# Kernel tuning notes

Hardware: AMD Instinct MI355X
Metric: run time of the kernel (lower is better)

## Reference

```python
import jax, jax.numpy as jnp
import numpy as np


def setup_inputs() -> dict:
    key = jax.random.key(0)
    ks = jax.random.split(key, 6)
    b, l, d, n, r = 2, 2048, 512, 64, 32
    x = jax.random.normal(ks[0], (b, l, d), dtype=jnp.float32)
    # x_proj: Linear(d, r + 2n, bias=False) -> weight (r+2n, d)
    W_xproj = jax.random.normal(ks[1], (r + 2 * n, d), dtype=jnp.float32) / np.sqrt(d)
    # dt_proj: Linear(r, d, bias=True)
    W_dt = jax.random.normal(ks[2], (d, r), dtype=jnp.float32) / np.sqrt(r)
    b_dt = jax.random.normal(ks[3], (d,), dtype=jnp.float32) * 0.01
    # A_log = log(repeat(arange(1, n+1), 'n -> d n'))
    A_log = jnp.log(jnp.broadcast_to(jnp.arange(1, n + 1, dtype=jnp.float32), (d, n)))
    D = jnp.ones((d,), dtype=jnp.float32)
    return {"x": x, "W_xproj": W_xproj, "W_dt": W_dt, "b_dt": b_dt, "A_log": A_log, "D": D}


def _s6_forward(x, W_xproj, W_dt, b_dt, A_log, D):
    d, n = A_log.shape
    r = W_dt.shape[1]
    A = -jnp.exp(A_log)                               # (d, n)
    x_dbl = jnp.einsum('bld,ed->ble', x, W_xproj)     # (b, l, r+2n)
    delta_r = x_dbl[..., :r]
    B = x_dbl[..., r:r + n]                           # (b, l, n)
    C = x_dbl[..., r + n:]                            # (b, l, n)
    delta = jax.nn.softplus(jnp.einsum('blr,dr->bld', delta_r, W_dt) + b_dt)  # (b, l, d)
    # discretize
    deltaA = jnp.exp(jnp.einsum('bld,dn->bldn', delta, A))        # (b, l, d, n)
    deltaB_u = jnp.einsum('bld,bln,bld->bldn', delta, B, x)       # (b, l, d, n)
    bsz = x.shape[0]
    h0 = jnp.zeros((bsz, d, n), dtype=x.dtype)

    def step(h, inp):
        dA_t, dBu_t, C_t = inp                        # (b,d,n), (b,d,n), (b,n)
        h = dA_t * h + dBu_t
        y_t = jnp.einsum('bdn,bn->bd', h, C_t)
        return h, y_t

    xs = (jnp.moveaxis(deltaA, 1, 0), jnp.moveaxis(deltaB_u, 1, 0), jnp.moveaxis(C, 1, 0))
    _, ys = jax.lax.scan(step, h0, xs)                # ys: (l, b, d)
    y = jnp.moveaxis(ys, 0, 1)                        # (b, l, d)
    return y + x * D


def reference(x, W_xproj, W_dt, b_dt, A_log, D):
    return _s6_forward(x, W_xproj, W_dt, b_dt, A_log, D)
```

## Files before the change

### kernel.cpp

```cpp
#include <hip/hip_runtime.h>
#include <cstdint>

#define Bsz 2
#define Lsz 2048
#define Dm  512
#define Nst 64
#define Rr  32
#define Ee  160
#define NCHUNK 64
#define CLEN   32
#define L2E 1.44269504f
#define LN2 0.69314718f

typedef __bf16  bf16x8 __attribute__((ext_vector_type(8)));
typedef float   f32x4  __attribute__((ext_vector_type(4)));
typedef unsigned short u16x8 __attribute__((ext_vector_type(8)));

__device__ __forceinline__ float rdlane(float v, int l) {
    return __int_as_float(__builtin_amdgcn_readlane(__float_as_int(v), l));
}
__device__ __forceinline__ float fexp2(float x) { return __builtin_amdgcn_exp2f(x); }
__device__ __forceinline__ float flog2(float x) { return __builtin_amdgcn_logf(x); }
__device__ __forceinline__ uint32_t bf16r(float f) {
    uint32_t u = __float_as_uint(f);
    u += 0x7FFFu + ((u >> 16) & 1u);
    return u >> 16;
}

__global__ __launch_bounds__(256) void kcast2(const float* __restrict__ a,
                                              unsigned short* __restrict__ oa, int na8,
                                              const float* __restrict__ b,
                                              unsigned short* __restrict__ ob, int nb8) {
    int gid = blockIdx.x * 256 + threadIdx.x;
    const float* in; unsigned short* op; int idx;
    if (gid < na8) { in = a; op = oa; idx = gid; }
    else { idx = gid - na8; if (idx >= nb8) return; in = b; op = ob; }
    const float4* ip = reinterpret_cast<const float4*>(in) + (size_t)idx * 2;
    float4 v0 = ip[0], v1 = ip[1];
    float vv[8] = {v0.x, v0.y, v0.z, v0.w, v1.x, v1.y, v1.z, v1.w};
    u16x8 r;
    #pragma unroll
    for (int j = 0; j < 8; ++j) r[j] = (unsigned short)bf16r(vv[j]);
    *reinterpret_cast<u16x8*>(op + (size_t)idx * 8) = r;
}

__global__ __launch_bounds__(256) void k1_mfma(const unsigned short* __restrict__ xbf,
                                               const unsigned short* __restrict__ wbf,
                                               float* __restrict__ xdbl) {
    const int tid = threadIdx.x;
    const int wv = tid >> 6, lane = tid & 63;
    const int ng = blockIdx.x % 10, mg = blockIdx.x / 10;
    const int m0 = mg * 64 + wv * 16;
    const int n0 = ng * 16;
    const int ra = lane & 15, kg = lane >> 4;
    const unsigned short* ap = xbf + (size_t)(m0 + ra) * Dm + kg * 8;
    const unsigned short* bp = wbf + (size_t)(n0 + ra) * Dm + kg * 8;
    f32x4 acc = {0.f, 0.f, 0.f, 0.f};
    #pragma unroll
    for (int ks = 0; ks < 16; ++ks) {
        bf16x8 a = *reinterpret_cast<const bf16x8*>(ap + ks * 32);
        bf16x8 b = *reinterpret_cast<const bf16x8*>(bp + ks * 32);
        acc = __builtin_amdgcn_mfma_f32_16x16x32_bf16(a, b, acc, 0, 0, 0);
    }
    float* dp = xdbl + (size_t)(m0 + kg * 4) * Ee + n0 + ra;
    dp[0]      = acc[0];
    dp[Ee]     = acc[1];
    dp[2 * Ee] = acc[2];
    dp[3 * Ee] = acc[3];
}

__global__ __launch_bounds__(256) void k2_delta(const float* __restrict__ xdbl,
                                                const float* __restrict__ x,
                                                const float* __restrict__ Wdt,
                                                const float* __restrict__ bdt,
                                                float* __restrict__ ddt,
                                                float* __restrict__ sumdl) {
    __shared__ float dr[64][33];
    __shared__ float wd[64][32];
    __shared__ float pt[64][65];
    const int tid = threadIdx.x;
    const int lt = blockIdx.x & 31;
    const int dt = (blockIdx.x >> 5) & 7;
    const int b  = blockIdx.x >> 8;
    const int l0 = lt * 64, d0 = dt * 64;

    for (int i = tid; i < 512; i += 256) {
        int l = i >> 3, j4 = i & 7;
        const float4 v = *reinterpret_cast<const float4*>(
            xdbl + (size_t)(b * Lsz + l0 + l) * Ee + j4 * 4);
        dr[l][j4 * 4 + 0] = v.x; dr[l][j4 * 4 + 1] = v.y;
        dr[l][j4 * 4 + 2] = v.z; dr[l][j4 * 4 + 3] = v.w;
    }
    for (int i = tid; i < 512; i += 256) {
        int dd = i >> 3, j4 = i & 7;
        *reinterpret_cast<float4*>(&wd[dd][j4 * 4]) =
            *reinterpret_cast<const float4*>(Wdt + (size_t)(d0 + dd) * Rr + j4 * 4);
    }
    __syncthreads();

    const int w = tid >> 6, lane = tid & 63;
    float drr[32];
    #pragma unroll
    for (int j = 0; j < 32; ++j) drr[j] = dr[lane][j];

    float xv[16];
    {
        const float* xp = x + (size_t)(b * Lsz + l0 + lane) * Dm + d0 + w * 16;
        #pragma unroll
        for (int q = 0; q < 4; ++q) {
            float4 v = reinterpret_cast<const float4*>(xp)[q];
            xv[q*4] = v.x; xv[q*4+1] = v.y; xv[q*4+2] = v.z; xv[q*4+3] = v.w;
        }
    }

    float dl[16];
    #pragma unroll
    for (int i = 0; i < 16; ++i) {
        int dd = w * 16 + i;
        float z = bdt[d0 + dd];
        const float4* wr = reinterpret_cast<const float4*>(&wd[dd][0]);
        #pragma unroll
        for (int j4 = 0; j4 < 8; ++j4) {
            float4 wv = wr[j4];
            z = fmaf(drr[j4*4+0], wv.x, z);
            z = fmaf(drr[j4*4+1], wv.y, z);
            z = fmaf(drr[j4*4+2], wv.z, z);
            z = fmaf(drr[j4*4+3], wv.w, z);
        }
        float t = fexp2(-fabsf(z) * L2E);
        dl[i] = fmaxf(z, 0.f) + flog2(1.f + t) * LN2;
    }

    #pragma unroll
    for (int i = 0; i < 16; ++i) {
        uint32_t db = bf16r(dl[i]);
        uint32_t ub = bf16r(dl[i] * xv[i]);
        pt[w * 16 + i][lane] = __uint_as_float(db | (ub << 16));
    }
    __syncthreads();
    for (int i = tid; i < 4096; i += 256) {
        int dd = i >> 6, ll = i & 63;
        ddt[((size_t)(b * Dm + d0 + dd)) * Lsz + l0 + ll] = pt[dd][ll];
    }
    if (tid < 64) {
        float s0 = 0.f, s1 = 0.f;
        #pragma unroll 16
        for (int q = 0; q < 32; ++q) {
            s0 += __uint_as_float(__float_as_uint(pt[tid][q]) << 16);
            s1 += __uint_as_float(__float_as_uint(pt[tid][32 + q]) << 16);
        }
        size_t sb = (size_t)(b * Dm + d0 + tid) * NCHUNK + lt * 2;
        sumdl[sb] = s0; sumdl[sb + 1] = s1;
    }
}

__global__ __launch_bounds__(256) void k3a(const float* __restrict__ ddt,
                                           const float* __restrict__ xdbl,
                                           const float* __restrict__ Alog,
                                           float* __restrict__ hf) {
    __shared__ float Bs[32][64];
    const int tid = threadIdx.x;
    const int w = __builtin_amdgcn_readfirstlane(tid >> 6);
    const int lane = tid & 63;
    const int c   = blockIdx.x & 63;
    const int grp = blockIdx.x >> 6;
    const int chan0 = grp * 32 + w * 8;
    const int b = chan0 >> 9;
    const int t0 = c * CLEN;
    const float* __restrict__ xb0 = xdbl + ((size_t)b * Lsz + t0) * Ee;
    for (int i = tid; i < 512; i += 256) {
        int row = i >> 4, q = i & 15;
        float4 v = *reinterpret_cast<const float4*>(xb0 + row * Ee + Rr + q * 4);
        *reinterpret_cast<float4*>(&Bs[row][q * 4]) = v;
    }
    const int tl = lane & 31;
    float A2[8], h[8], dpack[8];
    #pragma unroll
    for (int ch = 0; ch < 8; ++ch) {
        const int cc = chan0 + ch;
        A2[ch] = -expf(Alog[(size_t)(cc & 511) * Nst + lane]) * L2E;
        dpack[ch] = ddt[(size_t)cc * Lsz + t0 + tl];
        h[ch] = 0.f;
    }
    __syncthreads();
    #pragma unroll 8
    for (int j = 0; j < CLEN; ++j) {
        float Bv = Bs[j][lane];
        #pragma unroll
        for (int ch = 0; ch < 8; ++ch) {
            uint32_t wb = __float_as_uint(rdlane(dpack[ch], j));
            float sd = __uint_as_float(wb << 16);
            float su = __uint_as_float(wb & 0xffff0000u);
            h[ch] = fmaf(fexp2(sd * A2[ch]), h[ch], su * Bv);
        }
    }
    #pragma unroll
    for (int ch = 0; ch < 8; ++ch)
        hf[((size_t)(chan0 + ch) * NCHUNK + c) * Nst + lane] = h[ch];
}

__global__ __launch_bounds__(256) void k3b(const float* __restrict__ Alog,
                                           const float* __restrict__ sumdl,
                                           float* __restrict__ hf) {
    const int tid = threadIdx.x;
    const int w = tid >> 6, lane = tid & 63;
    const int chan = blockIdx.x * 4 + w;
    const int d = chan & 511;
    const float A2 = -expf(Alog[(size_t)d * Nst + lane]) * L2E;
    const float sv = sumdl[chan * NCHUNK + lane];
    const size_t base = (size_t)chan * NCHUNK * Nst + lane;
    float hv[8], nx[8];
    #pragma unroll
    for (int i = 0; i < 8; ++i) hv[i] = hf[base + i * Nst];
    float h0 = 0.f;
    for (int g = 0; g < 8; ++g) {
        if (g < 7) {
            #pragma unroll
            for (int i = 0; i < 8; ++i) nx[i] = hf[base + ((g + 1) * 8 + i) * Nst];
        }
        #pragma unroll
        for (int i = 0; i < 8; ++i) {
            const int c = g * 8 + i;
            float P = fexp2(A2 * rdlane(sv, c));
            hf[base + c * Nst] = h0;
            h0 = fmaf(P, h0, hv[i]);
        }
        #pragma unroll
        for (int i = 0; i < 8; ++i) hv[i] = nx[i];
    }
}

__global__ __launch_bounds__(256, 6) void k3c(const float* __restrict__ ddt,
                                              const float* __restrict__ xdbl,
                                              const float* __restrict__ Alog,
                                              const float* __restrict__ h0s,
                                              const float* __restrict__ x,
                                              const float* __restrict__ Dv,
                                              float* __restrict__ out) {
    __shared__ float BC[16][128];
    __shared__ float part[4][8][68];
    __shared__ float ystage[4][8][34];
    const int tid = threadIdx.x;
    const int w = __builtin_amdgcn_readfirstlane(tid >> 6);
    const int lane = tid & 63;
    const int c   = blockIdx.x & 63;
    const int grp = blockIdx.x >> 6;
    const int chan0 = grp * 32 + w * 8;
    const int b = chan0 >> 9;
    const int t0 = c * CLEN;
    const float* __restrict__ xb0 = xdbl + ((size_t)b * Lsz + t0) * Ee + Rr;

    const int tl = lane & 31;
    float A2[8], h[8], dpack[8];
    #pragma unroll
    for (int ch = 0; ch < 8; ++ch) {
        const int cc = chan0 + ch;
        A2[ch] = -expf(Alog[(size_t)(cc & 511) * Nst + lane]) * L2E;
        dpack[ch] = ddt[(size_t)cc * Lsz + t0 + tl];
        h[ch] = h0s[((size_t)cc * NCHUNK + c) * Nst + lane];
    }
    const int r8 = lane & 7, sg = lane >> 3;
    const int srow = tid >> 5, scol = (tid & 31) * 4;

    float4 pf0 = *reinterpret_cast<const float4*>(xb0 + srow * Ee + scol);
    float4 pf1 = *reinterpret_cast<const float4*>(xb0 + (srow + 8) * Ee + scol);

    for (int q = 0; q < 2; ++q) {
        __syncthreads();
        *reinterpret_cast<float4*>(&BC[srow][scol]) = pf0;
        *reinterpret_cast<float4*>(&BC[srow + 8][scol]) = pf1;
        if (q < 1) {
            pf0 = *reinterpret_cast<const float4*>(xb0 + (16 + srow) * Ee + scol);
            pf1 = *reinterpret_cast<const float4*>(xb0 + (16 + srow + 8) * Ee + scol);
        }
        __syncthreads();
        #pragma unroll
        for (int tt = 0; tt < 16; ++tt) {
            const int t = q * 16 + tt;
            float4 pa, pb;
            const bool doRed = (tt > 0) || (q > 0);
            if (doRed) {
                pa = *reinterpret_cast<const float4*>(&part[w][r8][sg * 8]);
                pb = *reinterpret_cast<const float4*>(&part[w][r8][sg * 8 + 4]);
            }
            float Bv = BC[tt][lane];
            float Cv = BC[tt][64 + lane];
            #pragma unroll
            for (int ch = 0; ch < 8; ++ch) {
                uint32_t wb = __float_as_uint(rdlane(dpack[ch], t));
                float sd = __uint_as_float(wb << 16);
                float su = __uint_as_float(wb & 0xffff0000u);
                h[ch] = fmaf(fexp2(sd * A2[ch]), h[ch], su * Bv);
                part[w][ch][lane] = h[ch] * Cv;
            }
            if (doRed) {
                float v = ((pa.x + pa.y) + (pa.z + pa.w)) + ((pb.x + pb.y) + (pb.z + pb.w));
                v += __shfl_xor(v, 8);
                v += __shfl_xor(v, 16);
                v += __shfl_xor(v, 32);
                if (lane < 8) ystage[w][lane][t - 1] = v;
            }
        }
    }
    {
        float4 pa = *reinterpret_cast<const float4*>(&part[w][r8][sg * 8]);
        float4 pb = *reinterpret_cast<const float4*>(&part[w][r8][sg * 8 + 4]);
        float v = ((pa.x + pa.y) + (pa.z + pa.w)) + ((pb.x + pb.y) + (pb.z + pb.w));
        v += __shfl_xor(v, 8); v += __shfl_xor(v, 16); v += __shfl_xor(v, 32);
        if (lane < 8) ystage[w][lane][31] = v;
    }
    __syncthreads();
    const int d0 = (grp * 32) & 511;
    for (int i = tid; i < 1024; i += 256) {
        int t = i >> 5, dd = i & 31;
        size_t gi = ((size_t)(b * Lsz + t0 + t)) * Dm + d0 + dd;
        out[gi] = ystage[dd >> 3][dd & 7][t] + x[gi] * Dv[d0 + dd];
    }
}

extern "C" void kernel_launch(void* const* d_in, const int* in_sizes, int n_in,
                              void* d_out, int out_size, void* d_ws, size_t ws_size,
                              hipStream_t stream) {
    const float* x    = (const float*)d_in[0];
    const float* Wxp  = (const float*)d_in[1];
    const float* Wdt  = (const float*)d_in[2];
    const float* bdt  = (const float*)d_in[3];
    const float* Alog = (const float*)d_in[4];
    const float* Dv   = (const float*)d_in[5];
    float* out = (float*)d_out;

    float* ws = (float*)d_ws;
    float*          xdbl    = ws;
    float*          hf      = ws + 655360;
    unsigned short* xbf     = (unsigned short*)(ws + 655360);
    unsigned short* wbf     = (unsigned short*)(ws + 1703936);
    float*          ddt     = ws + 4849664;
    float*          sumdl   = ws + 6946816;

    hipLaunchKernelGGL(kcast2,  dim3(1064), dim3(256), 0, stream, x, xbf, 262144, Wxp, wbf, 10240);
    hipLaunchKernelGGL(k1_mfma, dim3(640),  dim3(256), 0, stream, xbf, wbf, xdbl);
    hipLaunchKernelGGL(k2_delta,dim3(512),  dim3(256), 0, stream, xdbl, x, Wdt, bdt, ddt, sumdl);
    hipLaunchKernelGGL(k3a,     dim3(2048), dim3(256), 0, stream, ddt, xdbl, Alog, hf);
    hipLaunchKernelGGL(k3b,     dim3(256),  dim3(256), 0, stream, Alog, sumdl, hf);
    hipLaunchKernelGGL(k3c,     dim3(2048), dim3(256), 0, stream, ddt, xdbl, Alog, hf, x, Dv, out);
}
```

Baseline: 106.2 us.

## Pre-transpose B and C to bf16 per-chunk layout, load into registers in scans

```diff
diff --git a/kernel.cpp b/kernel.cpp
--- a/kernel.cpp
+++ b/kernel.cpp
@@ -25,6 +25,9 @@
     uint32_t u = __float_as_uint(f);
     u += 0x7FFFu + ((u >> 16) & 1u);
     return u >> 16;
+}
+__device__ __forceinline__ float bf2f(unsigned short v) {
+    return __uint_as_float((uint32_t)v << 16);
 }
 
 __global__ __launch_bounds__(256) void kcast2(const float* __restrict__ a,
@@ -74,7 +77,9 @@
                                                 const float* __restrict__ Wdt,
                                                 const float* __restrict__ bdt,
                                                 float* __restrict__ ddt,
-                                                float* __restrict__ sumdl) {
+                                                float* __restrict__ sumdl,
+                                                unsigned short* __restrict__ Bt,
+                                                unsigned short* __restrict__ Ct) {
     __shared__ float dr[64][33];
     __shared__ float wd[64][32];
     __shared__ float pt[64][65];
@@ -152,13 +157,36 @@
         size_t sb = (size_t)(b * Dm + d0 + tid) * NCHUNK + lt * 2;
         sumdl[sb] = s0; sumdl[sb + 1] = s1;
     }
+
+    if (dt == 0) {
+        #pragma unroll
+        for (int pass = 0; pass < 2; ++pass) {
+            __syncthreads();
+            for (int i = tid; i < 4096; i += 256) {
+                int l = i >> 6, e = i & 63;
+                pt[e][l] = xdbl[(size_t)(b * Lsz + l0 + l) * Ee + Rr + pass * 64 + e];
+            }
+            __syncthreads();
+            const int n = tid >> 2, q = tid & 3;
+            const int cc = lt * 2 + (q >> 1), tt0 = (q & 1) * 16;
+            unsigned short* dst = (pass ? Ct : Bt) +
+                (((size_t)b * NCHUNK + cc) * Nst + n) * CLEN + tt0;
+            u16x8 o0, o1;
+            #pragma unroll
+            for (int k = 0; k < 8; ++k) {
+                o0[k] = (unsigned short)bf16r(pt[n][(q & 1) * 16 + (q >> 1) * 32 + k]);
+                o1[k] = (unsigned short)bf16r(pt[n][(q & 1) * 16 + (q >> 1) * 32 + 8 + k]);
+            }
+            *reinterpret_cast<u16x8*>(dst)     = o0;
+            *reinterpret_cast<u16x8*>(dst + 8) = o1;
+        }
+    }
 }
 
 __global__ __launch_bounds__(256) void k3a(const float* __restrict__ ddt,
-                                           const float* __restrict__ xdbl,
+                                           const unsigned short* __restrict__ Bt,
                                            const float* __restrict__ Alog,
                                            float* __restrict__ hf) {
-    __shared__ float Bs[32][64];
     const int tid = threadIdx.x;
     const int w = __builtin_amdgcn_readfirstlane(tid >> 6);
     const int lane = tid & 63;
@@ -167,12 +195,11 @@
     const int chan0 = grp * 32 + w * 8;
     const int b = chan0 >> 9;
     const int t0 = c * CLEN;
-    const float* __restrict__ xb0 = xdbl + ((size_t)b * Lsz + t0) * Ee;
-    for (int i = tid; i < 512; i += 256) {
-        int row = i >> 4, q = i & 15;
-        float4 v = *reinterpret_cast<const float4*>(xb0 + row * Ee + Rr + q * 4);
-        *reinterpret_cast<float4*>(&Bs[row][q * 4]) = v;
-    }
+    const unsigned short* bp = Bt + (((size_t)b * NCHUNK + c) * Nst + lane) * CLEN;
+    u16x8 breg[4];
+    #pragma unroll
+    for (int i = 0; i < 4; ++i) breg[i] = *reinterpret_cast<const u16x8*>(bp + i * 8);
+
     const int tl = lane & 31;
     float A2[8], h[8], dpack[8];
     #pragma unroll
@@ -182,10 +209,9 @@
         dpack[ch] = ddt[(size_t)cc * Lsz + t0 + tl];
         h[ch] = 0.f;
     }
-    __syncthreads();
-    #pragma unroll 8
+    #pragma unroll
     for (int j = 0; j < CLEN; ++j) {
-        float Bv = Bs[j][lane];
+        float Bv = bf2f(breg[j >> 3][j & 7]);
         #pragma unroll
         for (int ch = 0; ch < 8; ++ch) {
             uint32_t wb = __float_as_uint(rdlane(dpack[ch], j));
@@ -231,13 +257,13 @@
 }
 
 __global__ __launch_bounds__(256, 6) void k3c(const float* __restrict__ ddt,
-                                              const float* __restrict__ xdbl,
+                                              const unsigned short* __restrict__ Bt,
+                                              const unsigned short* __restrict__ Ct,
                                               const float* __restrict__ Alog,
                                               const float* __restrict__ h0s,
                                               const float* __restrict__ x,
                                               const float* __restrict__ Dv,
                                               float* __restrict__ out) {
-    __shared__ float BC[16][128];
     __shared__ float part[4][8][68];
     __shared__ float ystage[4][8][34];
     const int tid = threadIdx.x;
@@ -248,7 +274,15 @@
     const int chan0 = grp * 32 + w * 8;
     const int b = chan0 >> 9;
     const int t0 = c * CLEN;
-    const float* __restrict__ xb0 = xdbl + ((size_t)b * Lsz + t0) * Ee + Rr;
+
+    const unsigned short* bp = Bt + (((size_t)b * NCHUNK + c) * Nst + lane) * CLEN;
+    const unsigned short* cp = Ct + (((size_t)b * NCHUNK + c) * Nst + lane) * CLEN;
+    u16x8 breg[4], creg[4];
+    #pragma unroll
+    for (int i = 0; i < 4; ++i) {
+        breg[i] = *reinterpret_cast<const u16x8*>(bp + i * 8);
+        creg[i] = *reinterpret_cast<const u16x8*>(cp + i * 8);
+    }
 
     const int tl = lane & 31;
     float A2[8], h[8], dpack[8];
@@ -260,46 +294,30 @@
         h[ch] = h0s[((size_t)cc * NCHUNK + c) * Nst + lane];
     }
     const int r8 = lane & 7, sg = lane >> 3;
-    const int srow = tid >> 5, scol = (tid & 31) * 4;
-
-    float4 pf0 = *reinterpret_cast<const float4*>(xb0 + srow * Ee + scol);
-    float4 pf1 = *reinterpret_cast<const float4*>(xb0 + (srow + 8) * Ee + scol);
-
-    for (int q = 0; q < 2; ++q) {
-        __syncthreads();
-        *reinterpret_cast<float4*>(&BC[srow][scol]) = pf0;
-        *reinterpret_cast<float4*>(&BC[srow + 8][scol]) = pf1;
-        if (q < 1) {
-            pf0 = *reinterpret_cast<const float4*>(xb0 + (16 + srow) * Ee + scol);
-            pf1 = *reinterpret_cast<const float4*>(xb0 + (16 + srow + 8) * Ee + scol);
-        }
-        __syncthreads();
-        #pragma unroll
-        for (int tt = 0; tt < 16; ++tt) {
-            const int t = q * 16 + tt;
-            float4 pa, pb;
-            const bool doRed = (tt > 0) || (q > 0);
-            if (doRed) {
-                pa = *reinterpret_cast<const float4*>(&part[w][r8][sg * 8]);
-                pb = *reinterpret_cast<const float4*>(&part[w][r8][sg * 8 + 4]);
-            }
-            float Bv = BC[tt][lane];
-            float Cv = BC[tt][64 + lane];
-            #pragma unroll
-            for (int ch = 0; ch < 8; ++ch) {
-                uint32_t wb = __float_as_uint(rdlane(dpack[ch], t));
-                float sd = __uint_as_float(wb << 16);
-                float su = __uint_as_float(wb & 0xffff0000u);
-                h[ch] = fmaf(fexp2(sd * A2[ch]), h[ch], su * Bv);
-                part[w][ch][lane] = h[ch] * Cv;
-            }
-            if (doRed) {
-                float v = ((pa.x + pa.y) + (pa.z + pa.w)) + ((pb.x + pb.y) + (pb.z + pb.w));
-                v += __shfl_xor(v, 8);
-                v += __shfl_xor(v, 16);
-                v += __shfl_xor(v, 32);
-                if (lane < 8) ystage[w][lane][t - 1] = v;
-            }
+
+    #pragma unroll
+    for (int t = 0; t < CLEN; ++t) {
+        float4 pa, pb;
+        if (t > 0) {
+            pa = *reinterpret_cast<const float4*>(&part[w][r8][sg * 8]);
+            pb = *reinterpret_cast<const float4*>(&part[w][r8][sg * 8 + 4]);
+        }
+        float Bv = bf2f(breg[t >> 3][t & 7]);
+        float Cv = bf2f(creg[t >> 3][t & 7]);
+        #pragma unroll
+        for (int ch = 0; ch < 8; ++ch) {
+            uint32_t wb = __float_as_uint(rdlane(dpack[ch], t));
+            float sd = __uint_as_float(wb << 16);
+            float su = __uint_as_float(wb & 0xffff0000u);
+            h[ch] = fmaf(fexp2(sd * A2[ch]), h[ch], su * Bv);
+            part[w][ch][lane] = h[ch] * Cv;
+        }
+        if (t > 0) {
+            float v = ((pa.x + pa.y) + (pa.z + pa.w)) + ((pb.x + pb.y) + (pb.z + pb.w));
+            v += __shfl_xor(v, 8);
+            v += __shfl_xor(v, 16);
+            v += __shfl_xor(v, 32);
+            if (lane < 8) ystage[w][lane][t - 1] = v;
         }
     }
     {
@@ -336,11 +354,13 @@
     unsigned short* wbf     = (unsigned short*)(ws + 1703936);
     float*          ddt     = ws + 4849664;
     float*          sumdl   = ws + 6946816;
+    unsigned short* Bt      = (unsigned short*)(ws + 7012352);
+    unsigned short* Ct      = (unsigned short*)(ws + 7143424);
 
     hipLaunchKernelGGL(kcast2,  dim3(1064), dim3(256), 0, stream, x, xbf, 262144, Wxp, wbf, 10240);
     hipLaunchKernelGGL(k1_mfma, dim3(640),  dim3(256), 0, stream, xbf, wbf, xdbl);
-    hipLaunchKernelGGL(k2_delta,dim3(512),  dim3(256), 0, stream, xdbl, x, Wdt, bdt, ddt, sumdl);
-    hipLaunchKernelGGL(k3a,     dim3(2048), dim3(256), 0, stream, ddt, xdbl, Alog, hf);
+    hipLaunchKernelGGL(k2_delta,dim3(512),  dim3(256), 0, stream, xdbl, x, Wdt, bdt, ddt, sumdl, Bt, Ct);
+    hipLaunchKernelGGL(k3a,     dim3(2048), dim3(256), 0, stream, ddt, Bt, Alog, hf);
     hipLaunchKernelGGL(k3b,     dim3(256),  dim3(256), 0, stream, Alog, sumdl, hf);
-    hipLaunchKernelGGL(k3c,     dim3(2048), dim3(256), 0, stream, ddt, xdbl, Alog, hf, x, Dv, out);
-}
+    hipLaunchKernelGGL(k3c,     dim3(2048), dim3(256), 0, stream, ddt, Bt, Ct, Alog, hf, x, Dv, out);
+}
```

Measured after the change: 106.5 us. No clear change (+0.3%).
